# Optimization experiments

Hardware: AMD Instinct MI355X
Metric: run time of the kernel (lower is better)

Reference implementation:

```python
import jax, jax.numpy as jnp
import numpy as np

B = 65536        # batch_size
F = 128          # feature_dim (shared-layer output)
H = 256          # hidden dim of each domain tower
D = 8            # num_domains
OUT = 1          # per-domain tower output dim


def setup_inputs() -> dict:
    key = jax.random.key(0)
    k_x, k_w1, k_b1, k_w2, k_b2, k_id = jax.random.split(key, 6)
    x = jax.random.normal(k_x, (B, F), dtype=jnp.float32)
    select_domain_ids = jax.random.randint(k_id, (B,), 0, D)
    # stacked per-domain MLP params (one tower per domain)
    s1 = 1.0 / np.sqrt(F)
    s2 = 1.0 / np.sqrt(H)
    W1 = jax.random.uniform(k_w1, (D, F, H), minval=-s1, maxval=s1, dtype=jnp.float32)
    b1 = jax.random.uniform(k_b1, (D, H), minval=-s1, maxval=s1, dtype=jnp.float32)
    W2 = jax.random.uniform(k_w2, (D, H, OUT), minval=-s2, maxval=s2, dtype=jnp.float32)
    b2 = jax.random.uniform(k_b2, (D, OUT), minval=-s2, maxval=s2, dtype=jnp.float32)
    return {"x": x, "select_domain_ids": select_domain_ids,
            "W1": W1, "b1": b1, "W2": W2, "b2": b2}


def reference(x, select_domain_ids, W1, b1, W2, b2):
    # Run EVERY domain tower on the full batch (dense compute), as the
    # original module does, then gather the selected domain per sample.
    h = jax.nn.relu(jnp.einsum('bf,dfh->bdh', x, W1) + b1)      # [B, D, H]
    logits = jnp.einsum('bdh,dho->bdo', h, W2) + b2             # [B, D, OUT]
    # domain_select: logits[arange(B), domain_ids] -> [B, OUT]
    out = jnp.take_along_axis(logits, select_domain_ids[:, None, None], axis=1)[:, 0]
    return out
```

## Files before the change

kernel.cpp:

```cpp
#include <hip/hip_runtime.h>
#include <hip/hip_bf16.h>

#define BN 65536
#define FD 128
#define HD 256
#define DN 8
#define NB 256
#define TM 64
#define SLOTS 8192
#define GRID_MAIN 1024

typedef float f32x4 __attribute__((ext_vector_type(4)));
using bf16x8 = __attribute__((ext_vector_type(8))) __bf16;
typedef unsigned short us4 __attribute__((ext_vector_type(4)));

__device__ __forceinline__ unsigned short f2bf(float f) {
  unsigned int x = __float_as_uint(f);
  x += 0x7fffu + ((x >> 16) & 1u);
  return (unsigned short)(x >> 16);
}

__global__ __launch_bounds__(256) void kA(
    const float* __restrict__ W1, const int* __restrict__ ids,
    unsigned short* __restrict__ W1T, int* __restrict__ cnt_blk) {
  __shared__ int hist[DN];
  __shared__ unsigned short tile[64][136];
  int t = threadIdx.x, bid = blockIdx.x;
  if (bid < NB) {
    if (t < DN) hist[t] = 0;
    __syncthreads();
    atomicAdd(&hist[ids[bid * 256 + t]], 1);
    __syncthreads();
    if (t < DN) cnt_blk[bid * DN + t] = hist[t];
  } else {
    int db = (bid - NB) >> 2, hb = (bid - NB) & 3;
    int fr = t >> 4, hq = t & 15;
    const float* src = W1 + (size_t)db * FD * HD + hb * 64 + hq * 4;
#pragma unroll
    for (int jj = 0; jj < 8; jj++) {
      int f = fr + 16 * jj;
      f32x4 v = *(const f32x4*)(src + (size_t)f * HD);
#pragma unroll
      for (int e = 0; e < 4; e++) tile[hq * 4 + e][f] = f2bf(v[e]);
    }
    __syncthreads();
    unsigned short* dst = W1T + (size_t)db * HD * FD + (size_t)hb * 64 * FD;
    int h = t >> 2, c = t & 3;
#pragma unroll
    for (int j = 0; j < 4; j++) {
      int f = c * 32 + j * 8;
      *(us4*)(dst + h * FD + f)     = *(const us4*)&tile[h][f];
      *(us4*)(dst + h * FD + f + 4) = *(const us4*)&tile[h][f + 4];
    }
  }
}

__global__ __launch_bounds__(256) void kBC(
    const int* __restrict__ ids, const int* __restrict__ cnt_blk,
    int* __restrict__ g_cnt, int* __restrict__ perm) {
  __shared__ int s_before[DN], s_total[DN], hist[DN];
  int t = threadIdx.x, bid = blockIdx.x;
  int w = t >> 6, l = t & 63;
  int full0 = 0, full1 = 0, bef0 = 0, bef1 = 0;
#pragma unroll
  for (int j = 0; j < 4; j++) {
    int r = l * 4 + j;
    int2 v = *(const int2*)(cnt_blk + r * DN + 2 * w);
    full0 += v.x; full1 += v.y;
    if (r < bid) { bef0 += v.x; bef1 += v.y; }
  }
#pragma unroll
  for (int off = 1; off < 64; off <<= 1) {
    full0 += __shfl_xor(full0, off); full1 += __shfl_xor(full1, off);
    bef0  += __shfl_xor(bef0, off);  bef1  += __shfl_xor(bef1, off);
  }
  if (t < DN) hist[t] = 0;
  if (l == 0) {
    s_before[2 * w] = bef0; s_before[2 * w + 1] = bef1;
    s_total[2 * w] = full0; s_total[2 * w + 1] = full1;
  }
  __syncthreads();
  int i = bid * 256 + t;
  int id = ids[i];
  int lp = atomicAdd(&hist[id], 1);
  perm[(id << 16) + s_before[id] + lp] = i;
  if (bid == 0 && t < DN) g_cnt[t] = s_total[t];
}

__global__ __launch_bounds__(512, 4) void kmain(
    const float* __restrict__ x, const float* __restrict__ b1,
    const float* __restrict__ W2, const float* __restrict__ b2,
    const unsigned short* __restrict__ W1T, const int* __restrict__ perm,
    const int* __restrict__ g_cnt, float* __restrict__ out) {
  __shared__ unsigned short xs[TM * FD];
  __shared__ float s_red[TM][9];
  int t = threadIdx.x;
  int lane = t & 63, w = t >> 6;
  int lg = lane >> 4, lr = lane & 15;

  for (int s = blockIdx.x; s < SLOTS; s += GRID_MAIN) {
    int d = s & 7, k = s >> 3;
    int rows = g_cnt[d] - k * TM;
    if (rows <= 0) continue;
    rows = min(rows, TM);
    const int* pr = perm + (d << 16) + k * TM;
    const unsigned short* Wd = W1T + (size_t)d * HD * FD;

    float b1v[2], w2v[2];
    bf16x8 bfr[4][2];
#pragma unroll
    for (int nt = 0; nt < 2; nt++) {
      int col = w * 32 + nt * 16 + lr;
      b1v[nt] = b1[d * HD + col];
      w2v[nt] = W2[d * HD + col];
#pragma unroll
      for (int ks = 0; ks < 4; ks++)
        bfr[ks][nt] = *(const bf16x8*)(Wd + (size_t)col * FD + ks * 32 + lg * 8);
    }

    {
      int r = t >> 3, c8 = t & 7;
      int gi = pr[min(r, rows - 1)];
      const float* xr = x + (size_t)gi * FD;
      f32x4 v[4];
#pragma unroll
      for (int j = 0; j < 4; j++) v[j] = *(const f32x4*)(xr + (c8 + 8 * j) * 4);
#pragma unroll
      for (int j = 0; j < 4; j++) {
        int fc = c8 + 8 * j;
        int us = (r * FD + fc * 4) ^ ((r & 7) << 3);
        us4 wv;
        wv[0] = f2bf(v[j][0]); wv[1] = f2bf(v[j][1]);
        wv[2] = f2bf(v[j][2]); wv[3] = f2bf(v[j][3]);
        *(us4*)&xs[us] = wv;
      }
    }
    __syncthreads();

    f32x4 acc[4][2];
#pragma unroll
    for (int mf = 0; mf < 4; mf++)
#pragma unroll
      for (int nt = 0; nt < 2; nt++) acc[mf][nt] = (f32x4){0.f, 0.f, 0.f, 0.f};

#pragma unroll
    for (int ks = 0; ks < 4; ks++) {
      bf16x8 a[4];
#pragma unroll
      for (int mf = 0; mf < 4; mf++) {
        int row = mf * 16 + lr;
        int us = (row * FD + ks * 32 + lg * 8) ^ ((row & 7) << 3);
        a[mf] = *(const bf16x8*)&xs[us];
      }
#pragma unroll
      for (int nt = 0; nt < 2; nt++)
#pragma unroll
        for (int mf = 0; mf < 4; mf++)
          acc[mf][nt] = __builtin_amdgcn_mfma_f32_16x16x32_bf16(a[mf], bfr[ks][nt], acc[mf][nt], 0, 0, 0);
    }

    float part[4][4];
#pragma unroll
    for (int mf = 0; mf < 4; mf++)
#pragma unroll
      for (int q = 0; q < 4; q++) part[mf][q] = 0.f;
#pragma unroll
    for (int nt = 0; nt < 2; nt++)
#pragma unroll
      for (int mf = 0; mf < 4; mf++)
#pragma unroll
        for (int q = 0; q < 4; q++) {
          float h = acc[mf][nt][q] + b1v[nt];
          h = h > 0.f ? h : 0.f;
          part[mf][q] = fmaf(h, w2v[nt], part[mf][q]);
        }
#pragma unroll
    for (int off = 1; off < 16; off <<= 1)
#pragma unroll
      for (int mf = 0; mf < 4; mf++)
#pragma unroll
        for (int q = 0; q < 4; q++)
          part[mf][q] += __shfl_xor(part[mf][q], off);
    if (lr == 0) {
#pragma unroll
      for (int mf = 0; mf < 4; mf++)
#pragma unroll
        for (int q = 0; q < 4; q++)
          s_red[mf * 16 + lg * 4 + q][w] = part[mf][q];
    }
    __syncthreads();
    if (t < rows) {
      const float* sr = s_red[t];
      out[pr[t]] = sr[0] + sr[1] + sr[2] + sr[3] + sr[4] + sr[5] + sr[6] + sr[7]
                   + b2[d];
    }
    __syncthreads();
  }
}

extern "C" void kernel_launch(void* const* d_in, const int* in_sizes, int n_in,
                              void* d_out, int out_size, void* d_ws, size_t ws_size,
                              hipStream_t stream) {
  const float* x   = (const float*)d_in[0];
  const int*   ids = (const int*)d_in[1];
  const float* W1  = (const float*)d_in[2];
  const float* b1  = (const float*)d_in[3];
  const float* W2  = (const float*)d_in[4];
  const float* b2  = (const float*)d_in[5];
  float* out = (float*)d_out;

  int* ws_i = (int*)d_ws;
  int* cnt_blk = ws_i;
  int* g_cnt   = ws_i + 2048;
  int* perm    = ws_i + 4096;
  unsigned short* W1T = (unsigned short*)(ws_i + 4096 + DN * BN);

  hipLaunchKernelGGL(kA, dim3(NB + 32), dim3(256), 0, stream, W1, ids, W1T, cnt_blk);
  hipLaunchKernelGGL(kBC, dim3(NB), dim3(256), 0, stream, ids, cnt_blk, g_cnt, perm);
  hipLaunchKernelGGL(kmain, dim3(GRID_MAIN), dim3(512), 0, stream, x, b1, W2, b2,
                     W1T, perm, g_cnt, out);
}
```

Measured before the change: 100.1 us.

## Fuse domain histogram and permutation scatter using ballot ranking and global atomics

```diff
diff --git a/kernel.cpp b/kernel.cpp
--- a/kernel.cpp
+++ b/kernel.cpp
@@ -20,18 +20,38 @@
   return (unsigned short)(x >> 16);
 }
 
-__global__ __launch_bounds__(256) void kA(
+__global__ __launch_bounds__(256) void k_pre(
     const float* __restrict__ W1, const int* __restrict__ ids,
-    unsigned short* __restrict__ W1T, int* __restrict__ cnt_blk) {
-  __shared__ int hist[DN];
+    unsigned short* __restrict__ W1T, int* __restrict__ g_cnt,
+    int* __restrict__ perm) {
   __shared__ unsigned short tile[64][136];
+  __shared__ int wcnt[4][DN];
+  __shared__ int base[DN];
   int t = threadIdx.x, bid = blockIdx.x;
+
   if (bid < NB) {
-    if (t < DN) hist[t] = 0;
-    __syncthreads();
-    atomicAdd(&hist[ids[bid * 256 + t]], 1);
-    __syncthreads();
-    if (t < DN) cnt_blk[bid * DN + t] = hist[t];
+    int w = t >> 6, l = t & 63;
+    int i = bid * 256 + t;
+    int id = ids[i];
+    unsigned long long my_mask = 0;
+    int cnt_l = 0;
+#pragma unroll
+    for (int d = 0; d < DN; d++) {
+      unsigned long long bm = __ballot(id == d);
+      if (id == d) my_mask = bm;
+      if (l == d) cnt_l = __popcll(bm);
+    }
+    if (l < DN) wcnt[w][l] = cnt_l;
+    int rank = __popcll(my_mask & ((1ull << l) - 1ull));
+    __syncthreads();
+    if (t < DN) {
+      int s0 = wcnt[0][t], s1 = wcnt[1][t], s2 = wcnt[2][t], s3 = wcnt[3][t];
+      wcnt[0][t] = 0; wcnt[1][t] = s0; wcnt[2][t] = s0 + s1;
+      wcnt[3][t] = s0 + s1 + s2;
+      base[t] = atomicAdd(&g_cnt[t], s0 + s1 + s2 + s3);
+    }
+    __syncthreads();
+    perm[(id << 16) + base[id] + wcnt[w][id] + rank] = i;
   } else {
     int db = (bid - NB) >> 2, hb = (bid - NB) & 3;
     int fr = t >> 4, hq = t & 15;
@@ -53,38 +73,6 @@
       *(us4*)(dst + h * FD + f + 4) = *(const us4*)&tile[h][f + 4];
     }
   }
-}
-
-__global__ __launch_bounds__(256) void kBC(
-    const int* __restrict__ ids, const int* __restrict__ cnt_blk,
-    int* __restrict__ g_cnt, int* __restrict__ perm) {
-  __shared__ int s_before[DN], s_total[DN], hist[DN];
-  int t = threadIdx.x, bid = blockIdx.x;
-  int w = t >> 6, l = t & 63;
-  int full0 = 0, full1 = 0, bef0 = 0, bef1 = 0;
-#pragma unroll
-  for (int j = 0; j < 4; j++) {
-    int r = l * 4 + j;
-    int2 v = *(const int2*)(cnt_blk + r * DN + 2 * w);
-    full0 += v.x; full1 += v.y;
-    if (r < bid) { bef0 += v.x; bef1 += v.y; }
-  }
-#pragma unroll
-  for (int off = 1; off < 64; off <<= 1) {
-    full0 += __shfl_xor(full0, off); full1 += __shfl_xor(full1, off);
-    bef0  += __shfl_xor(bef0, off);  bef1  += __shfl_xor(bef1, off);
-  }
-  if (t < DN) hist[t] = 0;
-  if (l == 0) {
-    s_before[2 * w] = bef0; s_before[2 * w + 1] = bef1;
-    s_total[2 * w] = full0; s_total[2 * w + 1] = full1;
-  }
-  __syncthreads();
-  int i = bid * 256 + t;
-  int id = ids[i];
-  int lp = atomicAdd(&hist[id], 1);
-  perm[(id << 16) + s_before[id] + lp] = i;
-  if (bid == 0 && t < DN) g_cnt[t] = s_total[t];
 }
 
 __global__ __launch_bounds__(512, 4) void kmain(
@@ -210,13 +198,13 @@
   float* out = (float*)d_out;
 
   int* ws_i = (int*)d_ws;
-  int* cnt_blk = ws_i;
-  int* g_cnt   = ws_i + 2048;
-  int* perm    = ws_i + 4096;
+  int* g_cnt = ws_i;
+  int* perm  = ws_i + 4096;
   unsigned short* W1T = (unsigned short*)(ws_i + 4096 + DN * BN);
 
-  hipLaunchKernelGGL(kA, dim3(NB + 32), dim3(256), 0, stream, W1, ids, W1T, cnt_blk);
-  hipLaunchKernelGGL(kBC, dim3(NB), dim3(256), 0, stream, ids, cnt_blk, g_cnt, perm);
+  hipMemsetAsync(g_cnt, 0, DN * sizeof(int), stream);
+  hipLaunchKernelGGL(k_pre, dim3(NB + 32), dim3(256), 0, stream,
+                     W1, ids, W1T, g_cnt, perm);
   hipLaunchKernelGGL(kmain, dim3(GRID_MAIN), dim3(512), 0, stream, x, b1, W2, b2,
                      W1T, perm, g_cnt, out);
 }
```

New measurement: 101.1 us. About the same (+1.1%).
